# Optimization experiments

Hardware: AMD Instinct MI355X
Metric: run time of the kernel (lower is better)

## Reference

```python
import jax, jax.numpy as jnp
import numpy as np

TEMPERATURE = 0.07
HARD_NEG_WEIGHT = 0.5
MARGIN = 0.2
NUM_HARD_NEG = 3
BATCH = 8192
DIM = 256
NUM_CLASSES = 512


def setup_inputs() -> dict:
    key = jax.random.key(0)
    k1, k2 = jax.random.split(key)
    embeddings = jax.random.normal(k1, (BATCH, DIM), dtype=jnp.float32)
    labels = jax.random.randint(k2, (BATCH,), 0, NUM_CLASSES, dtype=jnp.int64)
    return {"embeddings": embeddings, "labels": labels}


def reference(embeddings, labels):
    B = embeddings.shape[0]
    dt = embeddings.dtype
    # L2 normalize (torch F.normalize with eps clamp)
    norm = jnp.maximum(jnp.linalg.norm(embeddings, axis=-1, keepdims=True), 1e-12)
    e = embeddings / norm
    sim = jnp.matmul(e, e.T) / TEMPERATURE  # [B, B]

    same = (labels[:, None] == labels[None, :]).astype(dt)
    eye = jnp.eye(B, dtype=dt)
    pos_mask = same - eye            # positives excluding self
    neg_mask = 1.0 - same            # negatives (diag is 0 since labels==labels)

    # basic InfoNCE-style loss (unnormalized exp, as in the original)
    exp_sim = jnp.exp(sim) * (1.0 - eye)
    pos_sim = (exp_sim * pos_mask).sum(axis=-1)
    all_sim = exp_sim.sum(axis=-1)
    basic = -jnp.log(pos_sim / (all_sim + 1e-10) + 1e-10)
    has_pos = pos_mask.sum(axis=-1) > 0
    hp = has_pos.astype(dt)
    n_hp = jnp.maximum(hp.sum(), 1.0)
    basic_loss = (basic * hp).sum() / n_hp

    # hard negative mining: top-k most similar negatives vs best positive
    neg_inf = -jnp.inf
    neg_sim = jnp.where(neg_mask > 0, sim, neg_inf)
    k = min(NUM_HARD_NEG, B - 1)
    hard_neg_mean = jax.lax.top_k(neg_sim, k)[0].mean(axis=-1)
    pos_max = jnp.where(pos_mask > 0, sim, neg_inf).max(axis=-1)
    h = jax.nn.relu(hard_neg_mean - pos_max + MARGIN)
    h = jnp.where(has_pos, h, 0.0)
    hard_loss = (h * hp).sum() / n_hp

    # margin ranking: max positive vs max negative
    max_neg = neg_sim.max(axis=-1)
    m = jax.nn.relu(max_neg - pos_max + MARGIN)
    valid = (pos_max > neg_inf) & (max_neg > neg_inf)
    v = valid.astype(dt)
    n_v = jnp.maximum(v.sum(), 1.0)
    margin_loss = jnp.where(v.sum() > 0, jnp.where(valid, m, 0.0).sum() / n_v, 0.0)

    total = basic_loss + HARD_NEG_WEIGHT * hard_loss + 0.1 * margin_loss
    return total
```

## Files before the change

### kernel.cpp

```cpp
#include <hip/hip_runtime.h>
#include <cstdint>
#include <cstddef>

#define BATCH  8192
#define DIM    256
#define NSTRIP 8
#define SCOLS  1024
#define MROWS  128
#define NTILE  64
#define NITER  (SCOLS/NTILE)

static constexpr float INV_T   = 1.0f / 0.07f;
static constexpr float EXP2_SC = 1.4426950408889634f / 0.07f;
static constexpr float MARGIN  = 0.2f;

typedef __attribute__((ext_vector_type(8))) short short8;
typedef __attribute__((ext_vector_type(4))) float f32x4;

__device__ __forceinline__ unsigned short f2bf(float f){
  unsigned int u = __float_as_uint(f);
  u += 0x7FFFu + ((u >> 16) & 1u);
  return (unsigned short)(u >> 16);
}

__device__ __forceinline__ void ins3(float& t0, float& t1, float& t2, float s){
  float m0 = fmaxf(t0, s); float r1 = fminf(t0, s); t0 = m0;
  float m1 = fmaxf(t1, r1); float r2 = fminf(t1, r1); t1 = m1;
  t2 = fmaxf(t2, r2);
}

__global__ void norm_cast_kernel(const float* __restrict__ emb,
                                 unsigned short* __restrict__ E,
                                 float* __restrict__ accum){
  if (blockIdx.x == 0 && threadIdx.x < 8) accum[threadIdx.x] = 0.0f;
  const int wave = threadIdx.x >> 6;
  const int lane = threadIdx.x & 63;
  const int row  = blockIdx.x * 4 + wave;
  const float4 v = *(const float4*)(emb + (size_t)row * DIM + lane * 4);
  float ss = v.x*v.x + v.y*v.y + v.z*v.z + v.w*v.w;
  #pragma unroll
  for (int m = 1; m < 64; m <<= 1) ss += __shfl_xor(ss, m, 64);
  float nrm = fmaxf(sqrtf(ss), 1e-12f);
  float inv = 1.0f / nrm;
  ushort4 o;
  o.x = f2bf(v.x * inv); o.y = f2bf(v.y * inv);
  o.z = f2bf(v.z * inv); o.w = f2bf(v.w * inv);
  *(ushort4*)(E + (size_t)row * DIM + lane * 4) = o;
}

__global__ __launch_bounds__(256, 2)
void sim_stats_kernel(const unsigned short* __restrict__ E,
                      const int* __restrict__ labels,
                      float* __restrict__ partials){
  const int strip = blockIdx.x;
  const int rb    = blockIdx.y * MROWS;
  const int cs    = strip * SCOLS;
  const int tid   = threadIdx.x;
  const int wave  = tid >> 6;
  const int lane  = tid & 63;
  const int l     = lane & 15;
  const int q     = lane >> 4;

  __shared__ short8 Bs[32 * 64];
  __shared__ int labs[SCOLS];

  for (int i = tid; i < SCOLS; i += 256) labs[i] = labels[cs + i];

  const int row0 = rb + wave * 32;

  short8 a[2][8];
  #pragma unroll
  for (int rt = 0; rt < 2; ++rt){
    const unsigned short* rp = E + (size_t)(row0 + rt*16 + l) * DIM + q * 8;
    #pragma unroll
    for (int kk = 0; kk < 8; ++kk)
      a[rt][kk] = *(const short8*)(rp + kk * 32);
  }

  int labr[2][4];
  #pragma unroll
  for (int rt = 0; rt < 2; ++rt)
    #pragma unroll
    for (int rr = 0; rr < 4; ++rr)
      labr[rt][rr] = labels[row0 + rt*16 + q*4 + rr];

  float all_s[8], pos_s[8], pos_m[8], t0[8], t1[8], t2[8];
  #pragma unroll
  for (int s = 0; s < 8; ++s){
    all_s[s] = 0.f; pos_s[s] = 0.f;
    pos_m[s] = -INFINITY; t0[s] = -INFINITY; t1[s] = -INFINITY; t2[s] = -INFINITY;
  }

  for (int it = 0; it < NITER; ++it){
    const int cb = cs + it * NTILE;
    __syncthreads();
    #pragma unroll
    for (int ci = 0; ci < 8; ++ci){
      const int c = wave * 8 + ci;
      const unsigned short* g = E + (size_t)(cb + lane) * DIM + c * 8;
      __builtin_amdgcn_global_load_lds(
        (const __attribute__((address_space(1))) unsigned int*)g,
        (__attribute__((address_space(3))) unsigned int*)&Bs[c * 64],
        16, 0, 0);
    }
    __syncthreads();

    #pragma unroll
    for (int t = 0; t < 4; ++t){
      const int gcol = cb + t * 16 + l;
      const int labc = labs[it * NTILE + t * 16 + l];
      f32x4 acc0 = {0.f,0.f,0.f,0.f};
      f32x4 acc1 = {0.f,0.f,0.f,0.f};
      #pragma unroll
      for (int kk = 0; kk < 8; ++kk){
        short8 b = Bs[(kk * 4 + q) * 64 + t * 16 + l];
        acc0 = __builtin_amdgcn_mfma_f32_16x16x32_bf16(a[0][kk], b, acc0, 0, 0, 0);
        acc1 = __builtin_amdgcn_mfma_f32_16x16x32_bf16(a[1][kk], b, acc1, 0, 0, 0);
      }
      #pragma unroll
      for (int rt = 0; rt < 2; ++rt){
        #pragma unroll
        for (int rr = 0; rr < 4; ++rr){
          const float d    = rt ? acc1[rr] : acc0[rr];
          const int   s    = rt * 4 + rr;
          const int   grow = row0 + rt * 16 + q * 4 + rr;
          const float sim  = d * INV_T;
          const float ex   = __builtin_amdgcn_exp2f(d * EXP2_SC);
          const bool same  = (labc == labr[rt][rr]);
          const bool self  = (gcol == grow);
          all_s[s] += self ? 0.f : ex;
          const bool ispos = same && !self;
          pos_s[s] += ispos ? ex : 0.f;
          pos_m[s]  = fmaxf(pos_m[s], ispos ? sim : -INFINITY);
          const float sn = same ? -INFINITY : sim;
          ins3(t0[s], t1[s], t2[s], sn);
        }
      }
    }
  }

  #pragma unroll
  for (int mask = 1; mask < 16; mask <<= 1){
    #pragma unroll
    for (int s = 0; s < 8; ++s){
      all_s[s] += __shfl_xor(all_s[s], mask, 64);
      pos_s[s] += __shfl_xor(pos_s[s], mask, 64);
      pos_m[s]  = fmaxf(pos_m[s], __shfl_xor(pos_m[s], mask, 64));
      float b0 = __shfl_xor(t0[s], mask, 64);
      float b1 = __shfl_xor(t1[s], mask, 64);
      float b2 = __shfl_xor(t2[s], mask, 64);
      ins3(t0[s], t1[s], t2[s], b0);
      ins3(t0[s], t1[s], t2[s], b1);
      ins3(t0[s], t1[s], t2[s], b2);
    }
  }

  if (l == 0){
    #pragma unroll
    for (int s = 0; s < 8; ++s){
      const int grow = row0 + (s >> 2) * 16 + q * 4 + (s & 3);
      float* p = partials + ((size_t)grow * NSTRIP + strip) * 6;
      p[0] = all_s[s]; p[1] = pos_s[s]; p[2] = pos_m[s];
      p[3] = t0[s];    p[4] = t1[s];    p[5] = t2[s];
    }
  }
}

__global__ void merge_kernel(const float* __restrict__ partials,
                             float* __restrict__ accum){
  const int row = blockIdx.x * 256 + threadIdx.x;
  float all_s = 0.f, pos_s = 0.f, pos_m = -INFINITY;
  float t0 = -INFINITY, t1 = -INFINITY, t2 = -INFINITY;
  #pragma unroll
  for (int s = 0; s < NSTRIP; ++s){
    const float* p = partials + ((size_t)row * NSTRIP + s) * 6;
    all_s += p[0]; pos_s += p[1];
    pos_m = fmaxf(pos_m, p[2]);
    ins3(t0, t1, t2, p[3]); ins3(t0, t1, t2, p[4]); ins3(t0, t1, t2, p[5]);
  }
  const bool has_pos = pos_m > -INFINITY;
  float vb = 0.f, vh = 0.f, vhp = 0.f, vm = 0.f, vv = 0.f;
  if (has_pos){
    vhp = 1.f;
    vb  = -logf(pos_s / (all_s + 1e-10f) + 1e-10f);
    const float hnm = (t0 + t1 + t2) * (1.f/3.f);
    vh  = fmaxf(hnm - pos_m + MARGIN, 0.f);
    if (t0 > -INFINITY){
      vv = 1.f;
      vm = fmaxf(t0 - pos_m + MARGIN, 0.f);
    }
  }
  float vals[5] = {vb, vh, vhp, vm, vv};
  #pragma unroll
  for (int m = 1; m < 64; m <<= 1)
    #pragma unroll
    for (int i = 0; i < 5; ++i) vals[i] += __shfl_xor(vals[i], m, 64);
  if ((threadIdx.x & 63) == 0){
    #pragma unroll
    for (int i = 0; i < 5; ++i) atomicAdd(&accum[i], vals[i]);
  }
}

__global__ void final_kernel(const float* __restrict__ accum,
                             float* __restrict__ out){
  if (threadIdx.x == 0){
    const float nhp   = fmaxf(accum[2], 1.f);
    const float basic = accum[0] / nhp;
    const float hard  = accum[1] / nhp;
    const float marg  = (accum[4] > 0.f) ? (accum[3] / fmaxf(accum[4], 1.f)) : 0.f;
    out[0] = basic + 0.5f * hard + 0.1f * marg;
  }
}

extern "C" void kernel_launch(void* const* d_in, const int* in_sizes, int n_in,
                              void* d_out, int out_size, void* d_ws, size_t ws_size,
                              hipStream_t stream){
  const float* emb  = (const float*)d_in[0];
  const int* labels = (const int*)d_in[1];
  float* out        = (float*)d_out;
  char* ws          = (char*)d_ws;

  unsigned short* E = (unsigned short*)ws;
  const size_t E_BYTES = (size_t)BATCH * DIM * 2;
  float* partials   = (float*)(ws + E_BYTES);
  const size_t P_BYTES = (size_t)BATCH * NSTRIP * 6 * sizeof(float);
  float* accum      = (float*)(ws + E_BYTES + P_BYTES);

  norm_cast_kernel<<<BATCH/4, 256, 0, stream>>>(emb, E, accum);
  sim_stats_kernel<<<dim3(NSTRIP, BATCH/MROWS), 256, 0, stream>>>(E, labels, partials);
  merge_kernel<<<BATCH/256, 256, 0, stream>>>(partials, accum);
  final_kernel<<<1, 64, 0, stream>>>(accum, out);
}
```

Baseline: 141.6 us.

## Use 512-thread blocks, wave-uniform fast path for non-matching tiles, SoA partials

Blocks grow to 512 threads covering 256 rows against 512-column strips, which doubles the column strips and halves the per-wave LDS load count. The epilogue gains a fast path: when the tile is off the diagonal and no lane in the wave has a label match, it only accumulates the exp and inserts the raw dot into the top-3, skipping the mask logic. Scaling by 1/T moves out of the inner loop into the merge kernel. The partials layout changes to structure-of-arrays so merge reads coalesce. The risks are divergence from the __any check and register pressure under launch_bounds(512,4).

```diff
diff --git a/kernel.cpp b/kernel.cpp
--- a/kernel.cpp
+++ b/kernel.cpp
@@ -4,11 +4,12 @@
 
 #define BATCH  8192
 #define DIM    256
-#define NSTRIP 8
-#define SCOLS  1024
-#define MROWS  128
+#define NSTRIP 16
+#define SCOLS  512
+#define MROWS  256
 #define NTILE  64
 #define NITER  (SCOLS/NTILE)
+#define NTHREADS 512
 
 static constexpr float INV_T   = 1.0f / 0.07f;
 static constexpr float EXP2_SC = 1.4426950408889634f / 0.07f;
@@ -48,7 +49,7 @@
   *(ushort4*)(E + (size_t)row * DIM + lane * 4) = o;
 }
 
-__global__ __launch_bounds__(256, 2)
+__global__ __launch_bounds__(NTHREADS, 4)
 void sim_stats_kernel(const unsigned short* __restrict__ E,
                       const int* __restrict__ labels,
                       float* __restrict__ partials){
@@ -64,7 +65,7 @@
   __shared__ short8 Bs[32 * 64];
   __shared__ int labs[SCOLS];
 
-  for (int i = tid; i < SCOLS; i += 256) labs[i] = labels[cs + i];
+  for (int i = tid; i < SCOLS; i += NTHREADS) labs[i] = labels[cs + i];
 
   const int row0 = rb + wave * 32;
 
@@ -95,8 +96,8 @@
     const int cb = cs + it * NTILE;
     __syncthreads();
     #pragma unroll
-    for (int ci = 0; ci < 8; ++ci){
-      const int c = wave * 8 + ci;
+    for (int ci = 0; ci < 4; ++ci){
+      const int c = wave * 4 + ci;
       const unsigned short* g = E + (size_t)(cb + lane) * DIM + c * 8;
       __builtin_amdgcn_global_load_lds(
         (const __attribute__((address_space(1))) unsigned int*)g,
@@ -107,7 +108,6 @@
 
     #pragma unroll
     for (int t = 0; t < 4; ++t){
-      const int gcol = cb + t * 16 + l;
       const int labc = labs[it * NTILE + t * 16 + l];
       f32x4 acc0 = {0.f,0.f,0.f,0.f};
       f32x4 acc1 = {0.f,0.f,0.f,0.f};
@@ -119,21 +119,25 @@
       }
       #pragma unroll
       for (int rt = 0; rt < 2; ++rt){
+        const bool diag = (cb + t * 16) == (row0 + rt * 16);
         #pragma unroll
         for (int rr = 0; rr < 4; ++rr){
-          const float d    = rt ? acc1[rr] : acc0[rr];
-          const int   s    = rt * 4 + rr;
-          const int   grow = row0 + rt * 16 + q * 4 + rr;
-          const float sim  = d * INV_T;
-          const float ex   = __builtin_amdgcn_exp2f(d * EXP2_SC);
-          const bool same  = (labc == labr[rt][rr]);
-          const bool self  = (gcol == grow);
-          all_s[s] += self ? 0.f : ex;
-          const bool ispos = same && !self;
-          pos_s[s] += ispos ? ex : 0.f;
-          pos_m[s]  = fmaxf(pos_m[s], ispos ? sim : -INFINITY);
-          const float sn = same ? -INFINITY : sim;
-          ins3(t0[s], t1[s], t2[s], sn);
+          const float d  = rt ? acc1[rr] : acc0[rr];
+          const int   s  = rt * 4 + rr;
+          const float ex = __builtin_amdgcn_exp2f(d * EXP2_SC);
+          const bool same = (labc == labr[rt][rr]);
+          if (diag || __any(same)){
+            const bool self  = diag && (l == (q * 4 + rr));
+            const bool ispos = same && !self;
+            all_s[s] += self ? 0.f : ex;
+            pos_s[s] += ispos ? ex : 0.f;
+            pos_m[s]  = fmaxf(pos_m[s], ispos ? d : -INFINITY);
+            const float sn = same ? -INFINITY : d;
+            ins3(t0[s], t1[s], t2[s], sn);
+          } else {
+            all_s[s] += ex;
+            ins3(t0[s], t1[s], t2[s], d);
+          }
         }
       }
     }
@@ -159,9 +163,13 @@
     #pragma unroll
     for (int s = 0; s < 8; ++s){
       const int grow = row0 + (s >> 2) * 16 + q * 4 + (s & 3);
-      float* p = partials + ((size_t)grow * NSTRIP + strip) * 6;
-      p[0] = all_s[s]; p[1] = pos_s[s]; p[2] = pos_m[s];
-      p[3] = t0[s];    p[4] = t1[s];    p[5] = t2[s];
+      float* p = partials + (size_t)(strip * 6) * BATCH + grow;
+      p[0]                   = all_s[s];
+      p[(size_t)BATCH]       = pos_s[s];
+      p[(size_t)2 * BATCH]   = pos_m[s];
+      p[(size_t)3 * BATCH]   = t0[s];
+      p[(size_t)4 * BATCH]   = t1[s];
+      p[(size_t)5 * BATCH]   = t2[s];
     }
   }
 }
@@ -173,11 +181,16 @@
   float t0 = -INFINITY, t1 = -INFINITY, t2 = -INFINITY;
   #pragma unroll
   for (int s = 0; s < NSTRIP; ++s){
-    const float* p = partials + ((size_t)row * NSTRIP + s) * 6;
-    all_s += p[0]; pos_s += p[1];
-    pos_m = fmaxf(pos_m, p[2]);
-    ins3(t0, t1, t2, p[3]); ins3(t0, t1, t2, p[4]); ins3(t0, t1, t2, p[5]);
-  }
+    const float* p = partials + (size_t)(s * 6) * BATCH + row;
+    all_s += p[0];
+    pos_s += p[(size_t)BATCH];
+    pos_m  = fmaxf(pos_m, p[(size_t)2 * BATCH]);
+    ins3(t0, t1, t2, p[(size_t)3 * BATCH]);
+    ins3(t0, t1, t2, p[(size_t)4 * BATCH]);
+    ins3(t0, t1, t2, p[(size_t)5 * BATCH]);
+  }
+  pos_m *= INV_T; t0 *= INV_T; t1 *= INV_T; t2 *= INV_T;
+
   const bool has_pos = pos_m > -INFINITY;
   float vb = 0.f, vh = 0.f, vhp = 0.f, vm = 0.f, vv = 0.f;
   if (has_pos){
@@ -223,11 +236,11 @@
   unsigned short* E = (unsigned short*)ws;
   const size_t E_BYTES = (size_t)BATCH * DIM * 2;
   float* partials   = (float*)(ws + E_BYTES);
-  const size_t P_BYTES = (size_t)BATCH * NSTRIP * 6 * sizeof(float);
+  const size_t P_BYTES = (size_t)NSTRIP * 6 * BATCH * sizeof(float);
   float* accum      = (float*)(ws + E_BYTES + P_BYTES);
 
   norm_cast_kernel<<<BATCH/4, 256, 0, stream>>>(emb, E, accum);
-  sim_stats_kernel<<<dim3(NSTRIP, BATCH/MROWS), 256, 0, stream>>>(E, labels, partials);
+  sim_stats_kernel<<<dim3(NSTRIP, BATCH/MROWS), NTHREADS, 0, stream>>>(E, labels, partials);
   merge_kernel<<<BATCH/256, 256, 0, stream>>>(partials, accum);
   final_kernel<<<1, 64, 0, stream>>>(accum, out);
 }
```

After: 380.9 us. 2.69x slower.
